# Kernel tuning notes

Measured on AMD Instinct MI355X. Metric: run time of the kernel, lower is better.

## Reference

```python
import jax, jax.numpy as jnp
import numpy as np

N = 20000      # nodes
E = 320000     # edges (avg degree 16)
S = 2          # extra feature axis (mean-pooled before fc)
IN = 128       # in_feats
H = 246        # n_hidden (must be 246 to match fc = Linear(246, 1))


def setup_inputs() -> dict:
    key = jax.random.key(0)
    ks = jax.random.split(key, 8)
    feat = jax.random.normal(ks[0], (N, S, IN), jnp.float32)
    src = jax.random.randint(ks[1], (E,), 0, N, jnp.int32)
    dst = jax.random.randint(ks[2], (E,), 0, N, jnp.int32)
    glorot = lambda k, shp, fan: jax.random.normal(k, shp, jnp.float32) / np.sqrt(fan).astype(np.float32)
    return {
        "features": feat,
        "src": src,
        "dst": dst,
        "W0": glorot(ks[3], (IN, H), IN), "b0": jnp.zeros((H,), jnp.float32),
        "W1": glorot(ks[4], (H, H), H),   "b1": jnp.zeros((H,), jnp.float32),
        "W2": glorot(ks[5], (H, H), H),   "b2": jnp.zeros((H,), jnp.float32),
        "fc_w": glorot(ks[6], (H, 1), H), "fc_b": jnp.zeros((1,), jnp.float32),
    }


def reference(features, src, dst, W0, b0, W1, b1, W2, b2, fc_w, fc_b):
    # DGL GraphConv, norm='both': h' = act( D_in^{-1/2} A D_out^{-1/2} h W + b )
    ones = jnp.ones((src.shape[0],), jnp.float32)
    out_deg = jax.ops.segment_sum(ones, src, num_segments=N)
    in_deg = jax.ops.segment_sum(ones, dst, num_segments=N)
    norm_out = jax.lax.rsqrt(jnp.maximum(out_deg, 1.0))[:, None, None]  # [N,1,1]
    norm_in = jax.lax.rsqrt(jnp.maximum(in_deg, 1.0))[:, None, None]

    def graph_conv(h, W, b):
        h = h * norm_out                                      # [N,S,F] scale by src-side norm
        agg = jax.ops.segment_sum(h[src], dst, num_segments=N)  # gather->scatter-add over edges
        agg = agg * norm_in
        return jax.nn.relu(agg @ W + b)

    h = graph_conv(features.astype(jnp.float32), W0, b0)
    # dropout between layers is identity in eval mode
    h = graph_conv(h, W1, b1)
    h = graph_conv(h, W2, b2)
    return h.mean(axis=1) @ fc_w + fc_b  # [N,1]
```

## Files before the change

### kernel.cpp

```cpp
#include <hip/hip_runtime.h>
#include <hip/hip_fp16.h>

#define NN 20000
#define NE 320000
#define SS 2
#define FIN 128
#define FH 246

typedef _Float16 f16x8 __attribute__((ext_vector_type(8)));
typedef float f32x4 __attribute__((ext_vector_type(4)));

__global__ void degree_kernel(const int* __restrict__ src, const int* __restrict__ dst,
                              int* __restrict__ deg_out, int* __restrict__ deg_in) {
    int e = blockIdx.x * blockDim.x + threadIdx.x;
    if (e < NE) {
        atomicAdd(&deg_out[src[e]], 1);
        atomicAdd(&deg_in[dst[e]], 1);
    }
}

__global__ void alloc_kernel(const int* __restrict__ deg_out, const int* __restrict__ deg_in,
                             float* __restrict__ norm_out, float* __restrict__ norm_in,
                             int* __restrict__ row_start, int* __restrict__ cursor,
                             int* __restrict__ counter) {
    __shared__ int smem[256];
    __shared__ int base_s;
    int tid = threadIdx.x;
    int i = blockIdx.x * 256 + tid;
    int v = (i < NN) ? deg_in[i] : 0;
    smem[tid] = v;
    __syncthreads();
    for (int off = 1; off < 256; off <<= 1) {
        int t = (tid >= off) ? smem[tid - off] : 0;
        __syncthreads();
        smem[tid] += t;
        __syncthreads();
    }
    int incl = smem[tid];
    if (tid == 0) base_s = atomicAdd(counter, smem[255]);
    __syncthreads();
    if (i < NN) {
        int excl = base_s + incl - v;
        row_start[i] = excl;
        cursor[i]    = excl;
        norm_out[i] = rsqrtf(fmaxf((float)deg_out[i], 1.0f));
        norm_in[i]  = rsqrtf(fmaxf((float)v, 1.0f));
    }
}

__global__ void scatter_kernel(const int* __restrict__ src, const int* __restrict__ dst,
                               int* __restrict__ cursor, int* __restrict__ sorted_src) {
    int e = blockIdx.x * blockDim.x + threadIdx.x;
    if (e < NE) {
        int d = dst[e];
        int pos = atomicAdd(&cursor[d], 1);
        sorted_src[pos] = src[e];
    }
}

__global__ void convert_w_all(const float* __restrict__ W0, const float* __restrict__ W1,
                              const float* __restrict__ W2,
                              ushort* __restrict__ Wh0, ushort* __restrict__ Wl0,
                              ushort* __restrict__ Wh1, ushort* __restrict__ Wl1,
                              ushort* __restrict__ Wh2, ushort* __restrict__ Wl2) {
    int n = blockIdx.x, k = threadIdx.x;
    const float* W; ushort* Wh; ushort* Wl; int K;
    if (blockIdx.y == 0)      { W = W0; Wh = Wh0; Wl = Wl0; K = FIN; }
    else if (blockIdx.y == 1) { W = W1; Wh = Wh1; Wl = Wl1; K = FH; }
    else                      { W = W2; Wh = Wh2; Wl = Wl2; K = FH; }
    float v = (k < K && n < 246) ? W[k * 246 + n] : 0.f;
    _Float16 h = (_Float16)v;
    _Float16 l = (_Float16)(v - (float)h);
    Wh[n * 256 + k] = *(ushort*)&h;
    Wl[n * 256 + k] = *(ushort*)&l;
}

__global__ void init_out(float* __restrict__ out, const float* __restrict__ fcb) {
    int i = blockIdx.x * 256 + threadIdx.x;
    if (i < NN) out[i] = fcb[0];
}

template<int F4ROW, int NCH>
__global__ void aggregate2(const float* __restrict__ h,
                           const int* __restrict__ row_start,
                           const int* __restrict__ deg_in,
                           const int* __restrict__ sorted_src,
                           const float* __restrict__ norm_out,
                           const float* __restrict__ norm_in,
                           ushort* __restrict__ Ah, ushort* __restrict__ Al) {
    int g  = threadIdx.x >> 4;
    int l  = threadIdx.x & 15;
    int cb = blockIdx.x & (NCH - 1);
    int nb = blockIdx.x / NCH;
    int n  = nb * 8 + g;
    if (n >= NN) return;
    int idx = cb * 16 + l;
    const float4* hv = (const float4*)h;
    int beg = row_start[n];
    int end = beg + deg_in[n];
    float4 acc = {0.f, 0.f, 0.f, 0.f};
    int i = beg;
    for (; i + 4 <= end; i += 4) {
        int s0 = sorted_src[i + 0];
        int s1 = sorted_src[i + 1];
        int s2 = sorted_src[i + 2];
        int s3 = sorted_src[i + 3];
        float n0 = norm_out[s0], n1 = norm_out[s1];
        float n2 = norm_out[s2], n3 = norm_out[s3];
        float4 v0 = hv[(size_t)s0 * F4ROW + idx];
        float4 v1 = hv[(size_t)s1 * F4ROW + idx];
        float4 v2 = hv[(size_t)s2 * F4ROW + idx];
        float4 v3 = hv[(size_t)s3 * F4ROW + idx];
        acc.x += v0.x * n0 + v1.x * n1 + v2.x * n2 + v3.x * n3;
        acc.y += v0.y * n0 + v1.y * n1 + v2.y * n2 + v3.y * n3;
        acc.z += v0.z * n0 + v1.z * n1 + v2.z * n2 + v3.z * n3;
        acc.w += v0.w * n0 + v1.w * n1 + v2.w * n2 + v3.w * n3;
    }
    for (; i < end; ++i) {
        int s = sorted_src[i];
        float nr = norm_out[s];
        float4 v = hv[(size_t)s * F4ROW + idx];
        acc.x += v.x * nr;
        acc.y += v.y * nr;
        acc.z += v.z * nr;
        acc.w += v.w * nr;
    }
    float ni = norm_in[n];
    float v[4] = {acc.x * ni, acc.y * ni, acc.z * ni, acc.w * ni};
    ushort hp[4], lp[4];
#pragma unroll
    for (int j = 0; j < 4; ++j) {
        _Float16 hh = (_Float16)v[j];
        _Float16 ll = (_Float16)(v[j] - (float)hh);
        hp[j] = *(ushort*)&hh;
        lp[j] = *(ushort*)&ll;
    }
    ((uint2*)Ah)[(size_t)n * F4ROW + idx] = *(uint2*)hp;
    ((uint2*)Al)[(size_t)n * F4ROW + idx] = *(uint2*)lp;
}

template<int KP, bool FUSE>
__global__ __launch_bounds__(256) void gemm_split(const ushort* __restrict__ Ah,
                                                  const ushort* __restrict__ Al,
                                                  const ushort* __restrict__ Wh,
                                                  const ushort* __restrict__ Wl,
                                                  const float* __restrict__ b,
                                                  void* __restrict__ outv,
                                                  const float* __restrict__ fcw) {
    constexpr int NT = KP / 32;
    constexpr int AS = KP / 8;
    __shared__ __align__(16) _Float16 Ah_s[64][40];
    __shared__ __align__(16) _Float16 Al_s[64][40];
    __shared__ __align__(16) _Float16 Bh_s[128][40];
    __shared__ __align__(16) _Float16 Bl_s[128][40];

    int tid  = threadIdx.x;
    int m0   = blockIdx.x * 64;
    int n0   = blockIdx.y * 128;
    int wave = tid >> 6, lane = tid & 63;
    int wm = wave >> 1, wn = wave & 1;
    int lr = lane & 15, quad = lane >> 4;

    f32x4 acc[2][4];
#pragma unroll
    for (int mi = 0; mi < 2; ++mi)
#pragma unroll
        for (int ni = 0; ni < 4; ++ni) acc[mi][ni] = {0.f, 0.f, 0.f, 0.f};

    int ar = tid >> 2;
    int aq = tid & 3;
    const uint4* Ahv = (const uint4*)Ah;
    const uint4* Alv = (const uint4*)Al;
    const uint4* Whv = (const uint4*)Wh;
    const uint4* Wlv = (const uint4*)Wl;

    for (int t0 = 0; t0 < NT; ++t0) {
        size_t abase = (size_t)(m0 + ar) * AS + t0 * 4 + aq;
        *(uint4*)&Ah_s[ar][aq * 8] = Ahv[abase];
        *(uint4*)&Al_s[ar][aq * 8] = Alv[abase];
#pragma unroll
        for (int it = 0; it < 2; ++it) {
            int f = it * 256 + tid;
            int rn = f >> 2, q = f & 3;
            size_t base = (size_t)(n0 + rn) * 32 + t0 * 4 + q;
            *(uint4*)&Bh_s[rn][q * 8] = Whv[base];
            *(uint4*)&Bl_s[rn][q * 8] = Wlv[base];
        }
        __syncthreads();

        f16x8 ah[2], al[2], bh[4], bl[4];
#pragma unroll
        for (int mi = 0; mi < 2; ++mi) {
            ah[mi] = *(const f16x8*)&Ah_s[wm * 32 + mi * 16 + lr][quad * 8];
            al[mi] = *(const f16x8*)&Al_s[wm * 32 + mi * 16 + lr][quad * 8];
        }
#pragma unroll
        for (int ni = 0; ni < 4; ++ni) {
            bh[ni] = *(const f16x8*)&Bh_s[wn * 64 + ni * 16 + lr][quad * 8];
            bl[ni] = *(const f16x8*)&Bl_s[wn * 64 + ni * 16 + lr][quad * 8];
        }
#pragma unroll
        for (int mi = 0; mi < 2; ++mi)
#pragma unroll
            for (int ni = 0; ni < 4; ++ni) {
                acc[mi][ni] = __builtin_amdgcn_mfma_f32_16x16x32_f16(ah[mi], bh[ni], acc[mi][ni], 0, 0, 0);
                acc[mi][ni] = __builtin_amdgcn_mfma_f32_16x16x32_f16(al[mi], bh[ni], acc[mi][ni], 0, 0, 0);
                acc[mi][ni] = __builtin_amdgcn_mfma_f32_16x16x32_f16(ah[mi], bl[ni], acc[mi][ni], 0, 0, 0);
            }
        __syncthreads();
    }

    if (FUSE) {
        float* out = (float*)outv;
#pragma unroll
        for (int mi = 0; mi < 2; ++mi) {
#pragma unroll
            for (int i = 0; i < 4; ++i) {
                float p = 0.f;
#pragma unroll
                for (int ni = 0; ni < 4; ++ni) {
                    int c = n0 + wn * 64 + ni * 16 + lr;
                    if (c < 246)
                        p += fmaxf(acc[mi][ni][i] + b[c], 0.f) * fcw[c];
                }
#pragma unroll
                for (int off = 8; off > 0; off >>= 1)
                    p += __shfl_down(p, off, 16);
                if (lr == 0) {
                    int m = m0 + wm * 32 + mi * 16 + quad * 4 + i;
                    atomicAdd(&out[m >> 1], 0.5f * p);
                }
            }
        }
    } else {
        float* outF = (float*)outv;
#pragma unroll
        for (int ni = 0; ni < 4; ++ni) {
            int c = n0 + wn * 64 + ni * 16 + lr;
            float bj = (c < 246) ? b[c] : 0.f;
#pragma unroll
            for (int mi = 0; mi < 2; ++mi)
#pragma unroll
                for (int i = 0; i < 4; ++i) {
                    int m = m0 + wm * 32 + mi * 16 + quad * 4 + i;
                    outF[(size_t)m * 256 + c] = fmaxf(acc[mi][ni][i] + bj, 0.f);
                }
        }
    }
}

extern "C" void kernel_launch(void* const* d_in, const int* in_sizes, int n_in,
                              void* d_out, int out_size, void* d_ws, size_t ws_size,
                              hipStream_t stream) {
    const float* feat = (const float*)d_in[0];
    const int*   src  = (const int*)d_in[1];
    const int*   dst  = (const int*)d_in[2];
    const float* W0   = (const float*)d_in[3];
    const float* b0   = (const float*)d_in[4];
    const float* W1   = (const float*)d_in[5];
    const float* b1   = (const float*)d_in[6];
    const float* W2   = (const float*)d_in[7];
    const float* b2   = (const float*)d_in[8];
    const float* fcw  = (const float*)d_in[9];
    const float* fcb  = (const float*)d_in[10];
    float* out = (float*)d_out;

    char* ws = (char*)d_ws;
    size_t off = 0;
    auto alloc = [&](size_t bytes) {
        void* p = ws + off;
        off = (off + bytes + 255) & ~(size_t)255;
        return p;
    };
    int*    deg_out_i = (int*)alloc((2 * NN + 64) * sizeof(int));
    int*    deg_in_i  = deg_out_i + NN;
    int*    counter   = deg_out_i + 2 * NN;
    int*    row_start = (int*)alloc(NN * sizeof(int));
    int*    cursor    = (int*)alloc(NN * sizeof(int));
    int*    sorted    = (int*)alloc(NE * sizeof(int));
    float*  norm_out  = (float*)alloc(NN * sizeof(float));
    float*  norm_in   = (float*)alloc(NN * sizeof(float));
    ushort* Wh0 = (ushort*)alloc(256 * 256 * sizeof(ushort));
    ushort* Wl0 = (ushort*)alloc(256 * 256 * sizeof(ushort));
    ushort* Wh1 = (ushort*)alloc(256 * 256 * sizeof(ushort));
    ushort* Wl1 = (ushort*)alloc(256 * 256 * sizeof(ushort));
    ushort* Wh2 = (ushort*)alloc(256 * 256 * sizeof(ushort));
    ushort* Wl2 = (ushort*)alloc(256 * 256 * sizeof(ushort));
    ushort* Ahb = (ushort*)alloc((size_t)NN * SS * 256 * sizeof(ushort));
    ushort* Alb = (ushort*)alloc((size_t)NN * SS * 256 * sizeof(ushort));
    float*  bufH = (float*)alloc((size_t)NN * SS * 256 * sizeof(float));

    hipMemsetAsync(deg_out_i, 0, (2 * NN + 1) * sizeof(int), stream);

    degree_kernel<<<(NE + 255) / 256, 256, 0, stream>>>(src, dst, deg_out_i, deg_in_i);
    alloc_kernel<<<(NN + 255) / 256, 256, 0, stream>>>(deg_out_i, deg_in_i, norm_out, norm_in,
                                                       row_start, cursor, counter);
    scatter_kernel<<<(NE + 255) / 256, 256, 0, stream>>>(src, dst, cursor, sorted);

    convert_w_all<<<dim3(256, 3), 256, 0, stream>>>(W0, W1, W2, Wh0, Wl0, Wh1, Wl1, Wh2, Wl2);
    init_out<<<(NN + 255) / 256, 256, 0, stream>>>(out, fcb);

    const int NB8 = (NN + 7) / 8;
    dim3 ggrid(NN * SS / 64, 2);

    aggregate2<64, 4><<<NB8 * 4, 128, 0, stream>>>(feat, row_start, deg_in_i, sorted,
                                                   norm_out, norm_in, Ahb, Alb);
    gemm_split<FIN, false><<<ggrid, 256, 0, stream>>>(Ahb, Alb, Wh0, Wl0, b0, bufH, fcw);

    aggregate2<128, 8><<<NB8 * 8, 128, 0, stream>>>(bufH, row_start, deg_in_i, sorted,
                                                    norm_out, norm_in, Ahb, Alb);
    gemm_split<256, false><<<ggrid, 256, 0, stream>>>(Ahb, Alb, Wh1, Wl1, b1, bufH, fcw);

    aggregate2<128, 8><<<NB8 * 8, 128, 0, stream>>>(bufH, row_start, deg_in_i, sorted,
                                                    norm_out, norm_in, Ahb, Alb);
    gemm_split<256, true><<<ggrid, 256, 0, stream>>>(Ahb, Alb, Wh2, Wl2, b2, out, fcw);
}
```

Measured before the change: 367.0 us.

## Pad CSR rows to multiples of four, use ushort indices, fold norm_out into GEMM

```diff
diff --git a/kernel.cpp b/kernel.cpp
--- a/kernel.cpp
+++ b/kernel.cpp
@@ -27,8 +27,9 @@
     __shared__ int base_s;
     int tid = threadIdx.x;
     int i = blockIdx.x * 256 + tid;
-    int v = (i < NN) ? deg_in[i] : 0;
-    smem[tid] = v;
+    int v  = (i < NN) ? deg_in[i] : 0;
+    int vp = (v + 3) & ~3;
+    smem[tid] = vp;
     __syncthreads();
     for (int off = 1; off < 256; off <<= 1) {
         int t = (tid >= off) ? smem[tid - off] : 0;
@@ -40,7 +41,7 @@
     if (tid == 0) base_s = atomicAdd(counter, smem[255]);
     __syncthreads();
     if (i < NN) {
-        int excl = base_s + incl - v;
+        int excl = base_s + incl - vp;
         row_start[i] = excl;
         cursor[i]    = excl;
         norm_out[i] = rsqrtf(fmaxf((float)deg_out[i], 1.0f));
@@ -49,12 +50,23 @@
 }
 
 __global__ void scatter_kernel(const int* __restrict__ src, const int* __restrict__ dst,
-                               int* __restrict__ cursor, int* __restrict__ sorted_src) {
+                               int* __restrict__ cursor, ushort* __restrict__ sorted_src) {
     int e = blockIdx.x * blockDim.x + threadIdx.x;
     if (e < NE) {
         int d = dst[e];
         int pos = atomicAdd(&cursor[d], 1);
-        sorted_src[pos] = src[e];
+        sorted_src[pos] = (ushort)src[e];
+    }
+}
+
+__global__ void pad_fill(const int* __restrict__ row_start, const int* __restrict__ deg_in,
+                         ushort* __restrict__ sorted_src) {
+    int n = blockIdx.x * 256 + threadIdx.x;
+    if (n < NN) {
+        int d = deg_in[n];
+        int beg = row_start[n] + d;
+        int end = row_start[n] + ((d + 3) & ~3);
+        for (int p = beg; p < end; ++p) sorted_src[p] = (ushort)NN;
     }
 }
 
@@ -75,16 +87,18 @@
     Wl[n * 256 + k] = *(ushort*)&l;
 }
 
-__global__ void init_out(float* __restrict__ out, const float* __restrict__ fcb) {
+__global__ void init_out(float* __restrict__ out, const float* __restrict__ fcb,
+                         float* __restrict__ norm_out) {
     int i = blockIdx.x * 256 + threadIdx.x;
     if (i < NN) out[i] = fcb[0];
-}
-
-template<int F4ROW, int NCH>
-__global__ void aggregate2(const float* __restrict__ h,
+    if (i == 0) norm_out[NN] = 0.f;
+}
+
+template<int F4ROW, int NCH, bool NORM>
+__global__ void aggregate4(const float* __restrict__ h,
                            const int* __restrict__ row_start,
                            const int* __restrict__ deg_in,
-                           const int* __restrict__ sorted_src,
+                           const ushort* __restrict__ sorted_src,
                            const float* __restrict__ norm_out,
                            const float* __restrict__ norm_in,
                            ushort* __restrict__ Ah, ushort* __restrict__ Al) {
@@ -97,33 +111,32 @@
     int idx = cb * 16 + l;
     const float4* hv = (const float4*)h;
     int beg = row_start[n];
-    int end = beg + deg_in[n];
+    int end = beg + ((deg_in[n] + 3) & ~3);
     float4 acc = {0.f, 0.f, 0.f, 0.f};
-    int i = beg;
-    for (; i + 4 <= end; i += 4) {
-        int s0 = sorted_src[i + 0];
-        int s1 = sorted_src[i + 1];
-        int s2 = sorted_src[i + 2];
-        int s3 = sorted_src[i + 3];
-        float n0 = norm_out[s0], n1 = norm_out[s1];
-        float n2 = norm_out[s2], n3 = norm_out[s3];
-        float4 v0 = hv[(size_t)s0 * F4ROW + idx];
-        float4 v1 = hv[(size_t)s1 * F4ROW + idx];
-        float4 v2 = hv[(size_t)s2 * F4ROW + idx];
-        float4 v3 = hv[(size_t)s3 * F4ROW + idx];
-        acc.x += v0.x * n0 + v1.x * n1 + v2.x * n2 + v3.x * n3;
-        acc.y += v0.y * n0 + v1.y * n1 + v2.y * n2 + v3.y * n3;
-        acc.z += v0.z * n0 + v1.z * n1 + v2.z * n2 + v3.z * n3;
-        acc.w += v0.w * n0 + v1.w * n1 + v2.w * n2 + v3.w * n3;
-    }
-    for (; i < end; ++i) {
-        int s = sorted_src[i];
-        float nr = norm_out[s];
-        float4 v = hv[(size_t)s * F4ROW + idx];
-        acc.x += v.x * nr;
-        acc.y += v.y * nr;
-        acc.z += v.z * nr;
-        acc.w += v.w * nr;
+    for (int i = beg; i < end; i += 4) {
+        ushort4 ss = *(const ushort4*)&sorted_src[i];
+        int s0 = ss.x, s1 = ss.y, s2 = ss.z, s3 = ss.w;
+        if (NORM) {
+            float n0 = norm_out[s0], n1 = norm_out[s1];
+            float n2 = norm_out[s2], n3 = norm_out[s3];
+            float4 v0 = hv[(size_t)(s0 < NN ? s0 : NN - 1) * F4ROW + idx];
+            float4 v1 = hv[(size_t)(s1 < NN ? s1 : NN - 1) * F4ROW + idx];
+            float4 v2 = hv[(size_t)(s2 < NN ? s2 : NN - 1) * F4ROW + idx];
+            float4 v3 = hv[(size_t)(s3 < NN ? s3 : NN - 1) * F4ROW + idx];
+            acc.x += v0.x * n0 + v1.x * n1 + v2.x * n2 + v3.x * n3;
+            acc.y += v0.y * n0 + v1.y * n1 + v2.y * n2 + v3.y * n3;
+            acc.z += v0.z * n0 + v1.z * n1 + v2.z * n2 + v3.z * n3;
+            acc.w += v0.w * n0 + v1.w * n1 + v2.w * n2 + v3.w * n3;
+        } else {
+            float4 v0 = hv[(size_t)s0 * F4ROW + idx];
+            float4 v1 = hv[(size_t)s1 * F4ROW + idx];
+            float4 v2 = hv[(size_t)s2 * F4ROW + idx];
+            float4 v3 = hv[(size_t)s3 * F4ROW + idx];
+            acc.x += v0.x + v1.x + v2.x + v3.x;
+            acc.y += v0.y + v1.y + v2.y + v3.y;
+            acc.z += v0.z + v1.z + v2.z + v3.z;
+            acc.w += v0.w + v1.w + v2.w + v3.w;
+        }
     }
     float ni = norm_in[n];
     float v[4] = {acc.x * ni, acc.y * ni, acc.z * ni, acc.w * ni};
@@ -146,7 +159,8 @@
                                                   const ushort* __restrict__ Wl,
                                                   const float* __restrict__ b,
                                                   void* __restrict__ outv,
-                                                  const float* __restrict__ fcw) {
+                                                  const float* __restrict__ fcw,
+                                                  const float* __restrict__ nrm) {
     constexpr int NT = KP / 32;
     constexpr int AS = KP / 8;
     __shared__ __align__(16) _Float16 Ah_s[64][40];
@@ -243,7 +257,8 @@
 #pragma unroll
                 for (int i = 0; i < 4; ++i) {
                     int m = m0 + wm * 32 + mi * 16 + quad * 4 + i;
-                    outF[(size_t)m * 256 + c] = fmaxf(acc[mi][ni][i] + bj, 0.f);
+                    float no = nrm[m >> 1];
+                    outF[(size_t)m * 256 + c] = fmaxf(acc[mi][ni][i] + bj, 0.f) * no;
                 }
         }
     }
@@ -277,8 +292,8 @@
     int*    counter   = deg_out_i + 2 * NN;
     int*    row_start = (int*)alloc(NN * sizeof(int));
     int*    cursor    = (int*)alloc(NN * sizeof(int));
-    int*    sorted    = (int*)alloc(NE * sizeof(int));
-    float*  norm_out  = (float*)alloc(NN * sizeof(float));
+    ushort* sorted    = (ushort*)alloc((NE + 3 * NN + 16) * sizeof(ushort));
+    float*  norm_out  = (float*)alloc((NN + 1) * sizeof(float));
     float*  norm_in   = (float*)alloc(NN * sizeof(float));
     ushort* Wh0 = (ushort*)alloc(256 * 256 * sizeof(ushort));
     ushort* Wl0 = (ushort*)alloc(256 * 256 * sizeof(ushort));
@@ -288,30 +303,32 @@
     ushort* Wl2 = (ushort*)alloc(256 * 256 * sizeof(ushort));
     ushort* Ahb = (ushort*)alloc((size_t)NN * SS * 256 * sizeof(ushort));
     ushort* Alb = (ushort*)alloc((size_t)NN * SS * 256 * sizeof(ushort));
-    float*  bufH = (float*)alloc((size_t)NN * SS * 256 * sizeof(float));
+    float*  bufH = (float*)alloc(((size_t)NN * SS * 256 + 512) * sizeof(float));
 
     hipMemsetAsync(deg_out_i, 0, (2 * NN + 1) * sizeof(int), stream);
+    hipMemsetAsync(bufH + (size_t)NN * 512, 0, 512 * sizeof(float), stream);
 
     degree_kernel<<<(NE + 255) / 256, 256, 0, stream>>>(src, dst, deg_out_i, deg_in_i);
     alloc_kernel<<<(NN + 255) / 256, 256, 0, stream>>>(deg_out_i, deg_in_i, norm_out, norm_in,
                                                        row_start, cursor, counter);
+    pad_fill<<<(NN + 255) / 256, 256, 0, stream>>>(row_start, deg_in_i, sorted);
     scatter_kernel<<<(NE + 255) / 256, 256, 0, stream>>>(src, dst, cursor, sorted);
 
     convert_w_all<<<dim3(256, 3), 256, 0, stream>>>(W0, W1, W2, Wh0, Wl0, Wh1, Wl1, Wh2, Wl2);
-    init_out<<<(NN + 255) / 256, 256, 0, stream>>>(out, fcb);
+    init_out<<<(NN + 255) / 256, 256, 0, stream>>>(out, fcb, norm_out);
 
     const int NB8 = (NN + 7) / 8;
     dim3 ggrid(NN * SS / 64, 2);
 
-    aggregate2<64, 4><<<NB8 * 4, 128, 0, stream>>>(feat, row_start, deg_in_i, sorted,
-                                                   norm_out, norm_in, Ahb, Alb);
-    gemm_split<FIN, false><<<ggrid, 256, 0, stream>>>(Ahb, Alb, Wh0, Wl0, b0, bufH, fcw);
-
-    aggregate2<128, 8><<<NB8 * 8, 128, 0, stream>>>(bufH, row_start, deg_in_i, sorted,
-                                                    norm_out, norm_in, Ahb, Alb);
-    gemm_split<256, false><<<ggrid, 256, 0, stream>>>(Ahb, Alb, Wh1, Wl1, b1, bufH, fcw);
-
-    aggregate2<128, 8><<<NB8 * 8, 128, 0, stream>>>(bufH, row_start, deg_in_i, sorted,
-                                                    norm_out, norm_in, Ahb, Alb);
-    gemm_split<256, true><<<ggrid, 256, 0, stream>>>(Ahb, Alb, Wh2, Wl2, b2, out, fcw);
-}
+    aggregate4<64, 4, true><<<NB8 * 4, 128, 0, stream>>>(feat, row_start, deg_in_i, sorted,
+                                                         norm_out, norm_in, Ahb, Alb);
+    gemm_split<FIN, false><<<ggrid, 256, 0, stream>>>(Ahb, Alb, Wh0, Wl0, b0, bufH, fcw, norm_out);
+
+    aggregate4<128, 8, false><<<NB8 * 8, 128, 0, stream>>>(bufH, row_start, deg_in_i, sorted,
+                                                           norm_out, norm_in, Ahb, Alb);
+    gemm_split<256, false><<<ggrid, 256, 0, stream>>>(Ahb, Alb, Wh1, Wl1, b1, bufH, fcw, norm_out);
+
+    aggregate4<128, 8, false><<<NB8 * 8, 128, 0, stream>>>(bufH, row_start, deg_in_i, sorted,
+                                                           norm_out, norm_in, Ahb, Alb);
+    gemm_split<256, true><<<ggrid, 256, 0, stream>>>(Ahb, Alb, Wh2, Wl2, b2, out, fcw, norm_out);
+}
```

Result: faster. 355.2 us (-3.2%).
